# Kernel tuning notes

Hardware: AMD Instinct MI355X
Metric: run time of the kernel (lower is better)

## Reference

```python
import jax, jax.numpy as jnp
import numpy as np

B, K, S, H = 2, 16, 1024, 256
FFN_RATIO = 1.5
D_IN = 3 * H                      # concat of head/tail/context
D_FF = int(D_IN * FFN_RATIO)      # 1152
NEG_INF = -jnp.inf


def setup_inputs() -> dict:
    key = jax.random.key(0)
    ks = jax.random.split(key, 8)
    cand_span_reps = jax.random.normal(ks[0], (B, K, H), dtype=jnp.float32)
    # spans with start < end, leaving room so many pairs have a 'between' gap
    starts = jax.random.randint(ks[1], (B, K), 0, S - 8)
    widths = jax.random.randint(ks[2], (B, K), 1, 6)
    cand_span_ids = jnp.stack([starts, starts + widths], axis=-1).astype(jnp.int64)
    token_reps = jax.random.normal(ks[3], (B, S, H), dtype=jnp.float32)
    token_masks = jnp.ones((B, S), dtype=bool)
    rel_masks = jnp.ones((B, K * K), dtype=bool)
    # FFNProjectionLayer params: Linear(3H -> D_FF) + ReLU + Dropout(0) + Linear(D_FF -> H)
    W1 = jax.random.normal(ks[4], (D_IN, D_FF), dtype=jnp.float32) / np.sqrt(D_IN)
    b1 = jnp.zeros((D_FF,), dtype=jnp.float32)
    W2 = jax.random.normal(ks[5], (D_FF, H), dtype=jnp.float32) / np.sqrt(D_FF)
    b2 = jnp.zeros((H,), dtype=jnp.float32)
    return dict(cand_span_reps=cand_span_reps, cand_span_ids=cand_span_ids,
                token_reps=token_reps, token_masks=token_masks, rel_masks=rel_masks,
                W1=W1, b1=b1, W2=W2, b2=b2)


def reference(cand_span_reps, cand_span_ids, token_reps, token_masks, rel_masks,
              W1, b1, W2, b2):
    b, k, h = cand_span_reps.shape
    s = token_reps.shape[1]
    head = jnp.broadcast_to(cand_span_reps[:, :, None, :], (b, k, k, h))
    tail = jnp.broadcast_to(cand_span_reps[:, None, :, :], (b, k, k, h))
    hs = cand_span_ids[:, :, 0][:, :, None]   # (b,k,1)
    he = cand_span_ids[:, :, 1][:, :, None]
    ts = cand_span_ids[:, :, 0][:, None, :]   # (b,1,k)
    te = cand_span_ids[:, :, 1][:, None, :]
    min_end = jnp.minimum(he, te)              # (b,k,k)
    max_start = jnp.maximum(hs, ts)
    valid_between = (min_end < max_start) & rel_masks.reshape(b, k, k)
    seq = jnp.arange(s)
    # (b,k,k,s) dynamic-range mask: tokens in [min_end, max_start)
    mask = ((seq[None, None, None, :] >= min_end[..., None]) &
            (seq[None, None, None, :] < max_start[..., None]) &
            valid_between[..., None] &
            token_masks[:, None, None, :])
    # (b,k,k,s,h) masked tensor, max-pool over tokens (matches torch masked_fill+max)
    masked = jnp.where(mask[..., None], token_reps[:, None, None, :, :], NEG_INF)
    ctx = jnp.max(masked, axis=3)
    # replace all-masked (-inf) pairs with 0 to keep outputs finite
    ctx = jnp.where(mask.any(axis=3)[..., None], ctx, 0.0)
    rel = jnp.concatenate([head, tail, ctx], axis=-1)        # (b,k,k,3h)
    hid = jax.nn.relu(rel @ W1 + b1)                          # dropout p=0 -> identity
    out = hid @ W2 + b2                                       # (b,k,k,h)
    return out.reshape(b, k * k, h)
```

## Files before the change

### kernel.cpp

```cpp
#include <hip/hip_runtime.h>
#include <hip/hip_bf16.h>
#include <float.h>

#define BB 2
#define KK 16
#define SS 1024
#define HH 256
#define D_IN 768
#define D_FF 1152
#define NPAIR (BB*KK*KK)

#define CH 16
#define NCH (SS/CH)

typedef __attribute__((ext_vector_type(8))) short short8;
typedef __attribute__((ext_vector_type(4))) float floatx4;

__device__ __forceinline__ unsigned short f2bf(float f) {
    union { float f; unsigned u; } v; v.f = f;
    unsigned r = v.u + 0x7fffu + ((v.u >> 16) & 1u);
    return (unsigned short)(r >> 16);
}
__device__ __forceinline__ float bf2f(unsigned short s) {
    union { unsigned u; float f; } v; v.u = ((unsigned)s) << 16;
    return v.f;
}

__device__ __forceinline__ float rmax_f32(const float* __restrict__ p, int n)
{
    float m0 = -FLT_MAX, m1 = -FLT_MAX, m2 = -FLT_MAX, m3 = -FLT_MAX;
    int t = 0;
    for (; t + 4 <= n; t += 4) {
        float a = p[(size_t)(t + 0) * HH];
        float b = p[(size_t)(t + 1) * HH];
        float c = p[(size_t)(t + 2) * HH];
        float d = p[(size_t)(t + 3) * HH];
        m0 = fmaxf(m0, a); m1 = fmaxf(m1, b);
        m2 = fmaxf(m2, c); m3 = fmaxf(m3, d);
    }
    for (; t < n; ++t) m0 = fmaxf(m0, p[(size_t)t * HH]);
    return fmaxf(fmaxf(m0, m1), fmaxf(m2, m3));
}
__device__ __forceinline__ float rmax_bf16(const unsigned short* __restrict__ p, int n)
{
    float m0 = -FLT_MAX, m1 = -FLT_MAX, m2 = -FLT_MAX, m3 = -FLT_MAX;
    int t = 0;
    for (; t + 4 <= n; t += 4) {
        float a = bf2f(p[(size_t)(t + 0) * HH]);
        float b = bf2f(p[(size_t)(t + 1) * HH]);
        float c = bf2f(p[(size_t)(t + 2) * HH]);
        float d = bf2f(p[(size_t)(t + 3) * HH]);
        m0 = fmaxf(m0, a); m1 = fmaxf(m1, b);
        m2 = fmaxf(m2, c); m3 = fmaxf(m3, d);
    }
    for (; t < n; ++t) m0 = fmaxf(m0, bf2f(p[(size_t)t * HH]));
    return fmaxf(fmaxf(m0, m1), fmaxf(m2, m3));
}

#define W1_TILES (24*36)
#define W2_TILES (36*8)
#define PREP_BLOCKS (W1_TILES + W2_TILES + BB*NCH)
__global__ void prep_kernel(const float* __restrict__ W1, unsigned short* __restrict__ Wt1,
                            const float* __restrict__ W2, unsigned short* __restrict__ Wt2,
                            const float* __restrict__ tok, unsigned short* __restrict__ cmax)
{
    int bid = blockIdx.x;
    if (bid < W1_TILES + W2_TILES) {
        __shared__ unsigned short t[32][33];
        const float* W; unsigned short* Wt; int Kd, Nd, tk, tn;
        if (bid < W1_TILES) { W = W1; Wt = Wt1; Kd = D_IN;  Nd = D_FF; tk = bid / 36; tn = bid % 36; }
        else { bid -= W1_TILES; W = W2; Wt = Wt2; Kd = D_FF; Nd = HH;  tk = bid / 8;  tn = bid % 8; }
        const int r = threadIdx.x >> 5;
        const int c = threadIdx.x & 31;
        #pragma unroll
        for (int rr = r; rr < 32; rr += 8)
            t[rr][c] = f2bf(W[(size_t)(tk * 32 + rr) * Nd + tn * 32 + c]);
        __syncthreads();
        #pragma unroll
        for (int rr = r; rr < 32; rr += 8)
            Wt[(size_t)(tn * 32 + rr) * Kd + tk * 32 + c] = t[c][rr];
    } else {
        bid -= W1_TILES + W2_TILES;
        const int b = bid >> 6;
        const int c = bid & 63;
        const int h = threadIdx.x;
        const float* p = tok + ((size_t)(b * SS + c * CH)) * HH + h;
        float m0 = -FLT_MAX, m1 = -FLT_MAX, m2 = -FLT_MAX, m3 = -FLT_MAX;
        #pragma unroll
        for (int t = 0; t < CH; t += 4) {
            float a  = p[(size_t)(t + 0) * HH];
            float bb = p[(size_t)(t + 1) * HH];
            float cc = p[(size_t)(t + 2) * HH];
            float d  = p[(size_t)(t + 3) * HH];
            m0 = fmaxf(m0, a); m1 = fmaxf(m1, bb);
            m2 = fmaxf(m2, cc); m3 = fmaxf(m3, d);
        }
        cmax[(size_t)(b * NCH + c) * HH + h] = f2bf(fmaxf(fmaxf(m0, m1), fmaxf(m2, m3)));
    }
}

__global__ void build_x_kernel(const float* __restrict__ reps,
                               const int*   __restrict__ ids,
                               const float* __restrict__ tok,
                               const unsigned short* __restrict__ cmax,
                               unsigned short* __restrict__ X)
{
    const int p = blockIdx.x;
    const int h = threadIdx.x;
    const int b = p >> 8;
    const int i = (p >> 4) & 15;
    const int j = p & 15;

    const bool is64 = (ids[1] == 0);
    int hs, he, ts, te;
    if (is64) {
        hs = ids[((b*KK + i)*2 + 0) * 2];
        he = ids[((b*KK + i)*2 + 1) * 2];
        ts = ids[((b*KK + j)*2 + 0) * 2];
        te = ids[((b*KK + j)*2 + 1) * 2];
    } else {
        hs = ids[(b*KK + i)*2 + 0];
        he = ids[(b*KK + i)*2 + 1];
        ts = ids[(b*KK + j)*2 + 0];
        te = ids[(b*KK + j)*2 + 1];
    }

    const int lo = min(he, te);
    const int hi = max(hs, ts);

    const float head = reps[(size_t)(b*KK + i)*HH + h];
    const float tail = reps[(size_t)(b*KK + j)*HH + h];

    float m;
    if (lo < hi) {
        const float* trow = tok  + (size_t)b * SS  * HH + h;
        const unsigned short* crow = cmax + (size_t)b * NCH * HH + h;
        const int csta = (lo + CH - 1) >> 4;
        const int cend = hi >> 4;
        if (csta < cend) {
            float mA = rmax_f32(trow + (size_t)lo * HH, csta * CH - lo);
            float mB = rmax_bf16(crow + (size_t)csta * HH, cend - csta);
            float mC = rmax_f32(trow + (size_t)(cend * CH) * HH, hi - cend * CH);
            m = fmaxf(fmaxf(mA, mB), mC);
        } else {
            m = rmax_f32(trow + (size_t)lo * HH, hi - lo);
        }
    } else {
        m = 0.0f;
    }

    unsigned short* xr = X + (size_t)p * D_IN;
    xr[h]        = f2bf(head);
    xr[HH + h]   = f2bf(tail);
    xr[2*HH + h] = f2bf(m);
}

__global__ __launch_bounds__(256)
void gemm1_kernel(const unsigned short* __restrict__ A,
                  const unsigned short* __restrict__ Bt,
                  const float* __restrict__ bias,
                  unsigned short* __restrict__ C)
{
    constexpr int K = D_IN, N = D_FF, BK = 64, LDKT = BK + 8;
    __shared__ unsigned short As[64 * LDKT];
    __shared__ unsigned short Bs[64 * LDKT];

    const int tid  = threadIdx.x;
    const int lane = tid & 63;
    const int wave = tid >> 6;
    const int wm   = wave & 1;
    const int wn   = wave >> 1;
    const int quad = lane >> 4;
    const int l16  = lane & 15;

    const int rowBase = blockIdx.y * 64;
    const int colBase = blockIdx.x * 64;

    int srow[2], scol[2];
    #pragma unroll
    for (int s = 0; s < 2; ++s) {
        const int lin = tid * 2 + s;
        srow[s] = lin >> 3;
        scol[s] = (lin & 7) * 8;
    }

    floatx4 acc00 = {0.f,0.f,0.f,0.f}, acc01 = acc00, acc10 = acc00, acc11 = acc00;

    short8 pa[2], pb[2];
    #pragma unroll
    for (int s = 0; s < 2; ++s) {
        pa[s] = *(const short8*)&A [(size_t)(rowBase + srow[s]) * K + scol[s]];
        pb[s] = *(const short8*)&Bt[(size_t)(colBase + srow[s]) * K + scol[s]];
    }

    for (int k0 = 0; k0 < K; k0 += BK) {
        #pragma unroll
        for (int s = 0; s < 2; ++s) {
            *(short8*)&As[srow[s] * LDKT + scol[s]] = pa[s];
            *(short8*)&Bs[srow[s] * LDKT + scol[s]] = pb[s];
        }
        __syncthreads();

        const int kn = k0 + BK;
        if (kn < K) {
            #pragma unroll
            for (int s = 0; s < 2; ++s) {
                pa[s] = *(const short8*)&A [(size_t)(rowBase + srow[s]) * K + kn + scol[s]];
                pb[s] = *(const short8*)&Bt[(size_t)(colBase + srow[s]) * K + kn + scol[s]];
            }
        }

        #pragma unroll
        for (int kk = 0; kk < 2; ++kk) {
            const int ko = kk * 32 + quad * 8;
            short8 a0 = *(const short8*)&As[(wm * 32      + l16) * LDKT + ko];
            short8 a1 = *(const short8*)&As[(wm * 32 + 16 + l16) * LDKT + ko];
            short8 b0 = *(const short8*)&Bs[(wn * 32      + l16) * LDKT + ko];
            short8 b1 = *(const short8*)&Bs[(wn * 32 + 16 + l16) * LDKT + ko];
            acc00 = __builtin_amdgcn_mfma_f32_16x16x32_bf16(a0, b0, acc00, 0, 0, 0);
            acc01 = __builtin_amdgcn_mfma_f32_16x16x32_bf16(a0, b1, acc01, 0, 0, 0);
            acc10 = __builtin_amdgcn_mfma_f32_16x16x32_bf16(a1, b0, acc10, 0, 0, 0);
            acc11 = __builtin_amdgcn_mfma_f32_16x16x32_bf16(a1, b1, acc11, 0, 0, 0);
        }
        __syncthreads();
    }

    floatx4 accs[2][2] = {{acc00, acc01}, {acc10, acc11}};
    #pragma unroll
    for (int mt = 0; mt < 2; ++mt)
        #pragma unroll
        for (int nt = 0; nt < 2; ++nt)
            #pragma unroll
            for (int r = 0; r < 4; ++r) {
                const int m = rowBase + wm * 32 + mt * 16 + quad * 4 + r;
                const int n = colBase + wn * 32 + nt * 16 + l16;
                float v = fmaxf(accs[mt][nt][r] + bias[n], 0.0f);
                C[(size_t)m * N + n] = f2bf(v);
            }
}

__global__ __launch_bounds__(256)
void gemm2_kernel(const unsigned short* __restrict__ A,
                  const unsigned short* __restrict__ Bt,
                  const float* __restrict__ bias,
                  float* __restrict__ C)
{
    constexpr int K = D_FF, N = HH, BK = 64, LDKT = BK + 8;
    __shared__ unsigned short As[32 * LDKT];
    __shared__ unsigned short Bs[32 * LDKT];

    const int tid  = threadIdx.x;
    const int lane = tid & 63;
    const int wave = tid >> 6;
    const int wm   = wave & 1;
    const int wn   = wave >> 1;
    const int quad = lane >> 4;
    const int l16  = lane & 15;

    const int rowBase = blockIdx.y * 32;
    const int colBase = blockIdx.x * 32;

    const int srow = tid >> 3;
    const int scol = (tid & 7) * 8;

    floatx4 acc = {0.f,0.f,0.f,0.f};

    short8 pa = *(const short8*)&A [(size_t)(rowBase + srow) * K + scol];
    short8 pb = *(const short8*)&Bt[(size_t)(colBase + srow) * K + scol];

    for (int k0 = 0; k0 < K; k0 += BK) {
        *(short8*)&As[srow * LDKT + scol] = pa;
        *(short8*)&Bs[srow * LDKT + scol] = pb;
        __syncthreads();

        const int kn = k0 + BK;
        if (kn < K) {
            pa = *(const short8*)&A [(size_t)(rowBase + srow) * K + kn + scol];
            pb = *(const short8*)&Bt[(size_t)(colBase + srow) * K + kn + scol];
        }

        #pragma unroll
        for (int kk = 0; kk < 2; ++kk) {
            const int ko = kk * 32 + quad * 8;
            short8 a = *(const short8*)&As[(wm * 16 + l16) * LDKT + ko];
            short8 b = *(const short8*)&Bs[(wn * 16 + l16) * LDKT + ko];
            acc = __builtin_amdgcn_mfma_f32_16x16x32_bf16(a, b, acc, 0, 0, 0);
        }
        __syncthreads();
    }

    #pragma unroll
    for (int r = 0; r < 4; ++r) {
        const int m = rowBase + wm * 16 + quad * 4 + r;
        const int n = colBase + wn * 16 + l16;
        C[(size_t)m * N + n] = acc[r] + bias[n];
    }
}

extern "C" void kernel_launch(void* const* d_in, const int* in_sizes, int n_in,
                              void* d_out, int out_size, void* d_ws, size_t ws_size,
                              hipStream_t stream)
{
    const float* reps = (const float*)d_in[0];
    const int*   ids  = (const int*)  d_in[1];
    const float* tok  = (const float*)d_in[2];
    const float* W1   = (const float*)d_in[5];
    const float* b1   = (const float*)d_in[6];
    const float* W2   = (const float*)d_in[7];
    const float* b2   = (const float*)d_in[8];
    float* out = (float*)d_out;

    char* wsb = (char*)d_ws;
    unsigned short* Wt1  = (unsigned short*)(wsb);
    unsigned short* Wt2  = (unsigned short*)(wsb + 1769472);
    unsigned short* cmax = (unsigned short*)(wsb + 2359296);
    unsigned short* X    = (unsigned short*)(wsb + 2424832);
    unsigned short* hid  = (unsigned short*)(wsb + 3211264);

    prep_kernel<<<PREP_BLOCKS, 256, 0, stream>>>(W1, Wt1, W2, Wt2, tok, cmax);

    build_x_kernel<<<NPAIR, HH, 0, stream>>>(reps, ids, tok, cmax, X);

    gemm1_kernel<<<dim3(D_FF / 64, NPAIR / 64), 256, 0, stream>>>(X, Wt1, b1, hid);

    gemm2_kernel<<<dim3(HH / 32, NPAIR / 32), 256, 0, stream>>>(hid, Wt2, b2, out);
}
```

Measured before the change: 100.6 us.

## Fuse prep, build, and both GEMMs into one cooperative persistent kernel

Replaces the four separate launches (weight transpose and token chunk-max, pair feature build, GEMM1, GEMM2) with a single cooperative kernel of 512 blocks. The stages are separated by grid-wide syncs, and each block loops over its share of the prep jobs. This removes the launch overhead and inter-kernel gaps between stages. The max-reduction helpers are also widened to eight independent accumulators for more memory-level parallelism. The costs are the grid.sync barriers, idle blocks in the GEMM phases, and a dependence on cooperative launch residency.

```diff
diff --git a/kernel.cpp b/kernel.cpp
--- a/kernel.cpp
+++ b/kernel.cpp
@@ -1,6 +1,9 @@
 #include <hip/hip_runtime.h>
 #include <hip/hip_bf16.h>
+#include <hip/hip_cooperative_groups.h>
 #include <float.h>
+
+namespace cg = cooperative_groups;
 
 #define BB 2
 #define KK 16
@@ -13,6 +16,12 @@
 #define CH 16
 #define NCH (SS/CH)
 
+#define W1_TILES (24*36)
+#define W2_TILES (36*8)
+#define NJOBS (W1_TILES + W2_TILES + BB*NCH)
+
+#define GRID_BLOCKS 512
+
 typedef __attribute__((ext_vector_type(8))) short short8;
 typedef __attribute__((ext_vector_type(4))) float floatx4;
 
@@ -26,274 +35,268 @@
     return v.f;
 }
 
-__device__ __forceinline__ float rmax_f32(const float* __restrict__ p, int n)
+__device__ __forceinline__ float rmax8_f32(const float* __restrict__ p, int n)
 {
-    float m0 = -FLT_MAX, m1 = -FLT_MAX, m2 = -FLT_MAX, m3 = -FLT_MAX;
+    float m0=-FLT_MAX,m1=-FLT_MAX,m2=-FLT_MAX,m3=-FLT_MAX,
+          m4=-FLT_MAX,m5=-FLT_MAX,m6=-FLT_MAX,m7=-FLT_MAX;
     int t = 0;
-    for (; t + 4 <= n; t += 4) {
-        float a = p[(size_t)(t + 0) * HH];
-        float b = p[(size_t)(t + 1) * HH];
-        float c = p[(size_t)(t + 2) * HH];
-        float d = p[(size_t)(t + 3) * HH];
-        m0 = fmaxf(m0, a); m1 = fmaxf(m1, b);
-        m2 = fmaxf(m2, c); m3 = fmaxf(m3, d);
-    }
-    for (; t < n; ++t) m0 = fmaxf(m0, p[(size_t)t * HH]);
-    return fmaxf(fmaxf(m0, m1), fmaxf(m2, m3));
-}
-__device__ __forceinline__ float rmax_bf16(const unsigned short* __restrict__ p, int n)
+    for (; t + 8 <= n; t += 8) {
+        float v0=p[(size_t)(t+0)*HH], v1=p[(size_t)(t+1)*HH];
+        float v2=p[(size_t)(t+2)*HH], v3=p[(size_t)(t+3)*HH];
+        float v4=p[(size_t)(t+4)*HH], v5=p[(size_t)(t+5)*HH];
+        float v6=p[(size_t)(t+6)*HH], v7=p[(size_t)(t+7)*HH];
+        m0=fmaxf(m0,v0); m1=fmaxf(m1,v1); m2=fmaxf(m2,v2); m3=fmaxf(m3,v3);
+        m4=fmaxf(m4,v4); m5=fmaxf(m5,v5); m6=fmaxf(m6,v6); m7=fmaxf(m7,v7);
+    }
+    for (; t < n; ++t) m0 = fmaxf(m0, p[(size_t)t*HH]);
+    m0=fmaxf(m0,m1); m2=fmaxf(m2,m3); m4=fmaxf(m4,m5); m6=fmaxf(m6,m7);
+    return fmaxf(fmaxf(m0,m2), fmaxf(m4,m6));
+}
+__device__ __forceinline__ float rmax8_bf16(const unsigned short* __restrict__ p, int n)
 {
-    float m0 = -FLT_MAX, m1 = -FLT_MAX, m2 = -FLT_MAX, m3 = -FLT_MAX;
+    float m0=-FLT_MAX,m1=-FLT_MAX,m2=-FLT_MAX,m3=-FLT_MAX,
+          m4=-FLT_MAX,m5=-FLT_MAX,m6=-FLT_MAX,m7=-FLT_MAX;
     int t = 0;
-    for (; t + 4 <= n; t += 4) {
-        float a = bf2f(p[(size_t)(t + 0) * HH]);
-        float b = bf2f(p[(size_t)(t + 1) * HH]);
-        float c = bf2f(p[(size_t)(t + 2) * HH]);
-        float d = bf2f(p[(size_t)(t + 3) * HH]);
-        m0 = fmaxf(m0, a); m1 = fmaxf(m1, b);
-        m2 = fmaxf(m2, c); m3 = fmaxf(m3, d);
-    }
-    for (; t < n; ++t) m0 = fmaxf(m0, bf2f(p[(size_t)t * HH]));
-    return fmaxf(fmaxf(m0, m1), fmaxf(m2, m3));
-}
-
-#define W1_TILES (24*36)
-#define W2_TILES (36*8)
-#define PREP_BLOCKS (W1_TILES + W2_TILES + BB*NCH)
-__global__ void prep_kernel(const float* __restrict__ W1, unsigned short* __restrict__ Wt1,
-                            const float* __restrict__ W2, unsigned short* __restrict__ Wt2,
-                            const float* __restrict__ tok, unsigned short* __restrict__ cmax)
+    for (; t + 8 <= n; t += 8) {
+        float v0=bf2f(p[(size_t)(t+0)*HH]), v1=bf2f(p[(size_t)(t+1)*HH]);
+        float v2=bf2f(p[(size_t)(t+2)*HH]), v3=bf2f(p[(size_t)(t+3)*HH]);
+        float v4=bf2f(p[(size_t)(t+4)*HH]), v5=bf2f(p[(size_t)(t+5)*HH]);
+        float v6=bf2f(p[(size_t)(t+6)*HH]), v7=bf2f(p[(size_t)(t+7)*HH]);
+        m0=fmaxf(m0,v0); m1=fmaxf(m1,v1); m2=fmaxf(m2,v2); m3=fmaxf(m3,v3);
+        m4=fmaxf(m4,v4); m5=fmaxf(m5,v5); m6=fmaxf(m6,v6); m7=fmaxf(m7,v7);
+    }
+    for (; t < n; ++t) m0 = fmaxf(m0, bf2f(p[(size_t)t*HH]));
+    m0=fmaxf(m0,m1); m2=fmaxf(m2,m3); m4=fmaxf(m4,m5); m6=fmaxf(m6,m7);
+    return fmaxf(fmaxf(m0,m2), fmaxf(m4,m6));
+}
+
+__global__ __launch_bounds__(256, 2)
+void mega_kernel(const float* __restrict__ W1, const float* __restrict__ W2,
+                 const float* __restrict__ tok, const float* __restrict__ reps,
+                 const int* __restrict__ ids,
+                 const float* __restrict__ b1, const float* __restrict__ b2,
+                 unsigned short* __restrict__ Wt1, unsigned short* __restrict__ Wt2,
+                 unsigned short* __restrict__ cmax, unsigned short* __restrict__ X,
+                 unsigned short* __restrict__ hid, float* __restrict__ out)
 {
-    int bid = blockIdx.x;
-    if (bid < W1_TILES + W2_TILES) {
-        __shared__ unsigned short t[32][33];
-        const float* W; unsigned short* Wt; int Kd, Nd, tk, tn;
-        if (bid < W1_TILES) { W = W1; Wt = Wt1; Kd = D_IN;  Nd = D_FF; tk = bid / 36; tn = bid % 36; }
-        else { bid -= W1_TILES; W = W2; Wt = Wt2; Kd = D_FF; Nd = HH;  tk = bid / 8;  tn = bid % 8; }
-        const int r = threadIdx.x >> 5;
-        const int c = threadIdx.x & 31;
-        #pragma unroll
-        for (int rr = r; rr < 32; rr += 8)
-            t[rr][c] = f2bf(W[(size_t)(tk * 32 + rr) * Nd + tn * 32 + c]);
-        __syncthreads();
-        #pragma unroll
-        for (int rr = r; rr < 32; rr += 8)
-            Wt[(size_t)(tn * 32 + rr) * Kd + tk * 32 + c] = t[c][rr];
-    } else {
-        bid -= W1_TILES + W2_TILES;
-        const int b = bid >> 6;
-        const int c = bid & 63;
-        const int h = threadIdx.x;
-        const float* p = tok + ((size_t)(b * SS + c * CH)) * HH + h;
-        float m0 = -FLT_MAX, m1 = -FLT_MAX, m2 = -FLT_MAX, m3 = -FLT_MAX;
-        #pragma unroll
-        for (int t = 0; t < CH; t += 4) {
-            float a  = p[(size_t)(t + 0) * HH];
-            float bb = p[(size_t)(t + 1) * HH];
-            float cc = p[(size_t)(t + 2) * HH];
-            float d  = p[(size_t)(t + 3) * HH];
-            m0 = fmaxf(m0, a); m1 = fmaxf(m1, bb);
-            m2 = fmaxf(m2, cc); m3 = fmaxf(m3, d);
-        }
-        cmax[(size_t)(b * NCH + c) * HH + h] = f2bf(fmaxf(fmaxf(m0, m1), fmaxf(m2, m3)));
-    }
-}
-
-__global__ void build_x_kernel(const float* __restrict__ reps,
-                               const int*   __restrict__ ids,
-                               const float* __restrict__ tok,
-                               const unsigned short* __restrict__ cmax,
-                               unsigned short* __restrict__ X)
-{
-    const int p = blockIdx.x;
-    const int h = threadIdx.x;
-    const int b = p >> 8;
-    const int i = (p >> 4) & 15;
-    const int j = p & 15;
-
-    const bool is64 = (ids[1] == 0);
-    int hs, he, ts, te;
-    if (is64) {
-        hs = ids[((b*KK + i)*2 + 0) * 2];
-        he = ids[((b*KK + i)*2 + 1) * 2];
-        ts = ids[((b*KK + j)*2 + 0) * 2];
-        te = ids[((b*KK + j)*2 + 1) * 2];
-    } else {
-        hs = ids[(b*KK + i)*2 + 0];
-        he = ids[(b*KK + i)*2 + 1];
-        ts = ids[(b*KK + j)*2 + 0];
-        te = ids[(b*KK + j)*2 + 1];
-    }
-
-    const int lo = min(he, te);
-    const int hi = max(hs, ts);
-
-    const float head = reps[(size_t)(b*KK + i)*HH + h];
-    const float tail = reps[(size_t)(b*KK + j)*HH + h];
-
-    float m;
-    if (lo < hi) {
-        const float* trow = tok  + (size_t)b * SS  * HH + h;
-        const unsigned short* crow = cmax + (size_t)b * NCH * HH + h;
-        const int csta = (lo + CH - 1) >> 4;
-        const int cend = hi >> 4;
-        if (csta < cend) {
-            float mA = rmax_f32(trow + (size_t)lo * HH, csta * CH - lo);
-            float mB = rmax_bf16(crow + (size_t)csta * HH, cend - csta);
-            float mC = rmax_f32(trow + (size_t)(cend * CH) * HH, hi - cend * CH);
-            m = fmaxf(fmaxf(mA, mB), mC);
-        } else {
-            m = rmax_f32(trow + (size_t)lo * HH, hi - lo);
-        }
-    } else {
-        m = 0.0f;
-    }
-
-    unsigned short* xr = X + (size_t)p * D_IN;
-    xr[h]        = f2bf(head);
-    xr[HH + h]   = f2bf(tail);
-    xr[2*HH + h] = f2bf(m);
-}
-
-__global__ __launch_bounds__(256)
-void gemm1_kernel(const unsigned short* __restrict__ A,
-                  const unsigned short* __restrict__ Bt,
-                  const float* __restrict__ bias,
-                  unsigned short* __restrict__ C)
-{
-    constexpr int K = D_IN, N = D_FF, BK = 64, LDKT = BK + 8;
-    __shared__ unsigned short As[64 * LDKT];
-    __shared__ unsigned short Bs[64 * LDKT];
-
-    const int tid  = threadIdx.x;
+    cg::grid_group grid = cg::this_grid();
+    __shared__ unsigned short smem[2 * 64 * 72];
+
+    const int bid = blockIdx.x;
+    const int tid = threadIdx.x;
     const int lane = tid & 63;
     const int wave = tid >> 6;
-    const int wm   = wave & 1;
-    const int wn   = wave >> 1;
     const int quad = lane >> 4;
     const int l16  = lane & 15;
 
-    const int rowBase = blockIdx.y * 64;
-    const int colBase = blockIdx.x * 64;
-
-    int srow[2], scol[2];
-    #pragma unroll
-    for (int s = 0; s < 2; ++s) {
-        const int lin = tid * 2 + s;
-        srow[s] = lin >> 3;
-        scol[s] = (lin & 7) * 8;
-    }
-
-    floatx4 acc00 = {0.f,0.f,0.f,0.f}, acc01 = acc00, acc10 = acc00, acc11 = acc00;
-
-    short8 pa[2], pb[2];
-    #pragma unroll
-    for (int s = 0; s < 2; ++s) {
-        pa[s] = *(const short8*)&A [(size_t)(rowBase + srow[s]) * K + scol[s]];
-        pb[s] = *(const short8*)&Bt[(size_t)(colBase + srow[s]) * K + scol[s]];
-    }
-
-    for (int k0 = 0; k0 < K; k0 += BK) {
+    for (int job = bid; job < NJOBS; job += GRID_BLOCKS) {
+        if (job < W1_TILES + W2_TILES) {
+            int jb = job;
+            const float* W; unsigned short* Wt; int Kd, Nd, tk, tn;
+            if (jb < W1_TILES) { W = W1; Wt = Wt1; Kd = D_IN;  Nd = D_FF; tk = jb / 36; tn = jb % 36; }
+            else { jb -= W1_TILES; W = W2; Wt = Wt2; Kd = D_FF; Nd = HH;  tk = jb / 8;  tn = jb % 8; }
+            unsigned short (*t)[33] = (unsigned short(*)[33])smem;
+            const int r = tid >> 5;
+            const int c = tid & 31;
+            #pragma unroll
+            for (int rr = r; rr < 32; rr += 8)
+                t[rr][c] = f2bf(W[(size_t)(tk * 32 + rr) * Nd + tn * 32 + c]);
+            __syncthreads();
+            #pragma unroll
+            for (int rr = r; rr < 32; rr += 8)
+                Wt[(size_t)(tn * 32 + rr) * Kd + tk * 32 + c] = t[c][rr];
+            __syncthreads();
+        } else {
+            const int jb = job - (W1_TILES + W2_TILES);
+            const int b = jb >> 6;
+            const int c = jb & 63;
+            const float* p = tok + ((size_t)(b * SS + c * CH)) * HH + tid;
+            float m0=-FLT_MAX,m1=-FLT_MAX,m2=-FLT_MAX,m3=-FLT_MAX;
+            #pragma unroll
+            for (int t = 0; t < CH; t += 4) {
+                float a  = p[(size_t)(t+0)*HH];
+                float bb = p[(size_t)(t+1)*HH];
+                float cc = p[(size_t)(t+2)*HH];
+                float d  = p[(size_t)(t+3)*HH];
+                m0=fmaxf(m0,a); m1=fmaxf(m1,bb); m2=fmaxf(m2,cc); m3=fmaxf(m3,d);
+            }
+            cmax[(size_t)(b * NCH + c) * HH + tid] =
+                f2bf(fmaxf(fmaxf(m0,m1), fmaxf(m2,m3)));
+        }
+    }
+
+    grid.sync();
+
+    {
+        const int p = bid;
+        const int b = p >> 8;
+        const int i = (p >> 4) & 15;
+        const int j = p & 15;
+        const int h = tid;
+
+        const bool is64 = (ids[1] == 0);
+        int hs, he, ts, te;
+        if (is64) {
+            hs = ids[((b*KK + i)*2 + 0) * 2];
+            he = ids[((b*KK + i)*2 + 1) * 2];
+            ts = ids[((b*KK + j)*2 + 0) * 2];
+            te = ids[((b*KK + j)*2 + 1) * 2];
+        } else {
+            hs = ids[(b*KK + i)*2 + 0];
+            he = ids[(b*KK + i)*2 + 1];
+            ts = ids[(b*KK + j)*2 + 0];
+            te = ids[(b*KK + j)*2 + 1];
+        }
+        const int lo = min(he, te);
+        const int hi = max(hs, ts);
+
+        const float head = reps[(size_t)(b*KK + i)*HH + h];
+        const float tail = reps[(size_t)(b*KK + j)*HH + h];
+
+        float m;
+        if (lo < hi) {
+            const float* trow = tok  + (size_t)b * SS  * HH + h;
+            const unsigned short* crow = cmax + (size_t)b * NCH * HH + h;
+            const int csta = (lo + CH - 1) >> 4;
+            const int cend = hi >> 4;
+            if (csta < cend) {
+                float mA = rmax8_f32(trow + (size_t)lo * HH, csta * CH - lo);
+                float mB = rmax8_bf16(crow + (size_t)csta * HH, cend - csta);
+                float mC = rmax8_f32(trow + (size_t)(cend * CH) * HH, hi - cend * CH);
+                m = fmaxf(fmaxf(mA, mB), mC);
+            } else {
+                m = rmax8_f32(trow + (size_t)lo * HH, hi - lo);
+            }
+        } else {
+            m = 0.0f;
+        }
+
+        unsigned short* xr = X + (size_t)p * D_IN;
+        xr[h]        = f2bf(head);
+        xr[HH + h]   = f2bf(tail);
+        xr[2*HH + h] = f2bf(m);
+    }
+
+    grid.sync();
+
+    if (bid < (D_FF/64) * (NPAIR/64)) {
+        constexpr int K = D_IN, N = D_FF, BK = 64, LDKT = BK + 8;
+        unsigned short* As = smem;
+        unsigned short* Bs = smem + 64 * LDKT;
+        const int wm = wave & 1;
+        const int wn = wave >> 1;
+        const int rowBase = (bid / (D_FF/64)) * 64;
+        const int colBase = (bid % (D_FF/64)) * 64;
+
+        int srow[2], scol[2];
         #pragma unroll
         for (int s = 0; s < 2; ++s) {
-            *(short8*)&As[srow[s] * LDKT + scol[s]] = pa[s];
-            *(short8*)&Bs[srow[s] * LDKT + scol[s]] = pb[s];
-        }
-        __syncthreads();
-
-        const int kn = k0 + BK;
-        if (kn < K) {
+            const int lin = tid * 2 + s;
+            srow[s] = lin >> 3;
+            scol[s] = (lin & 7) * 8;
+        }
+
+        floatx4 acc00 = {0.f,0.f,0.f,0.f}, acc01 = acc00, acc10 = acc00, acc11 = acc00;
+
+        short8 pa[2], pb[2];
+        #pragma unroll
+        for (int s = 0; s < 2; ++s) {
+            pa[s] = *(const short8*)&X  [(size_t)(rowBase + srow[s]) * K + scol[s]];
+            pb[s] = *(const short8*)&Wt1[(size_t)(colBase + srow[s]) * K + scol[s]];
+        }
+
+        for (int k0 = 0; k0 < K; k0 += BK) {
             #pragma unroll
             for (int s = 0; s < 2; ++s) {
-                pa[s] = *(const short8*)&A [(size_t)(rowBase + srow[s]) * K + kn + scol[s]];
-                pb[s] = *(const short8*)&Bt[(size_t)(colBase + srow[s]) * K + kn + scol[s]];
-            }
-        }
-
+                *(short8*)&As[srow[s] * LDKT + scol[s]] = pa[s];
+                *(short8*)&Bs[srow[s] * LDKT + scol[s]] = pb[s];
+            }
+            __syncthreads();
+
+            const int kn = k0 + BK;
+            if (kn < K) {
+                #pragma unroll
+                for (int s = 0; s < 2; ++s) {
+                    pa[s] = *(const short8*)&X  [(size_t)(rowBase + srow[s]) * K + kn + scol[s]];
+                    pb[s] = *(const short8*)&Wt1[(size_t)(colBase + srow[s]) * K + kn + scol[s]];
+                }
+            }
+
+            #pragma unroll
+            for (int kk = 0; kk < 2; ++kk) {
+                const int ko = kk * 32 + quad * 8;
+                short8 a0 = *(const short8*)&As[(wm * 32      + l16) * LDKT + ko];
+                short8 a1 = *(const short8*)&As[(wm * 32 + 16 + l16) * LDKT + ko];
+                short8 b0 = *(const short8*)&Bs[(wn * 32      + l16) * LDKT + ko];
+                short8 b1 = *(const short8*)&Bs[(wn * 32 + 16 + l16) * LDKT + ko];
+                acc00 = __builtin_amdgcn_mfma_f32_16x16x32_bf16(a0, b0, acc00, 0, 0, 0);
+                acc01 = __builtin_amdgcn_mfma_f32_16x16x32_bf16(a0, b1, acc01, 0, 0, 0);
+                acc10 = __builtin_amdgcn_mfma_f32_16x16x32_bf16(a1, b0, acc10, 0, 0, 0);
+                acc11 = __builtin_amdgcn_mfma_f32_16x16x32_bf16(a1, b1, acc11, 0, 0, 0);
+            }
+            __syncthreads();
+        }
+
+        floatx4 accs[2][2] = {{acc00, acc01}, {acc10, acc11}};
         #pragma unroll
-        for (int kk = 0; kk < 2; ++kk) {
-            const int ko = kk * 32 + quad * 8;
-            short8 a0 = *(const short8*)&As[(wm * 32      + l16) * LDKT + ko];
-            short8 a1 = *(const short8*)&As[(wm * 32 + 16 + l16) * LDKT + ko];
-            short8 b0 = *(const short8*)&Bs[(wn * 32      + l16) * LDKT + ko];
-            short8 b1 = *(const short8*)&Bs[(wn * 32 + 16 + l16) * LDKT + ko];
-            acc00 = __builtin_amdgcn_mfma_f32_16x16x32_bf16(a0, b0, acc00, 0, 0, 0);
-            acc01 = __builtin_amdgcn_mfma_f32_16x16x32_bf16(a0, b1, acc01, 0, 0, 0);
-            acc10 = __builtin_amdgcn_mfma_f32_16x16x32_bf16(a1, b0, acc10, 0, 0, 0);
-            acc11 = __builtin_amdgcn_mfma_f32_16x16x32_bf16(a1, b1, acc11, 0, 0, 0);
-        }
-        __syncthreads();
-    }
-
-    floatx4 accs[2][2] = {{acc00, acc01}, {acc10, acc11}};
-    #pragma unroll
-    for (int mt = 0; mt < 2; ++mt)
+        for (int mt = 0; mt < 2; ++mt)
+            #pragma unroll
+            for (int nt = 0; nt < 2; ++nt)
+                #pragma unroll
+                for (int r = 0; r < 4; ++r) {
+                    const int m = rowBase + wm * 32 + mt * 16 + quad * 4 + r;
+                    const int n = colBase + wn * 32 + nt * 16 + l16;
+                    float v = fmaxf(accs[mt][nt][r] + b1[n], 0.0f);
+                    hid[(size_t)m * N + n] = f2bf(v);
+                }
+    }
+
+    grid.sync();
+
+    if (bid < (HH/32) * (NPAIR/32)) {
+        constexpr int K = D_FF, N = HH, BK = 64, LDKT = BK + 8;
+        unsigned short* As = smem;
+        unsigned short* Bs = smem + 32 * LDKT;
+        const int wm = wave & 1;
+        const int wn = wave >> 1;
+        const int rowBase = (bid / (HH/32)) * 32;
+        const int colBase = (bid % (HH/32)) * 32;
+
+        const int srow = tid >> 3;
+        const int scol = (tid & 7) * 8;
+
+        floatx4 acc = {0.f,0.f,0.f,0.f};
+
+        short8 pa = *(const short8*)&hid[(size_t)(rowBase + srow) * K + scol];
+        short8 pb = *(const short8*)&Wt2[(size_t)(colBase + srow) * K + scol];
+
+        for (int k0 = 0; k0 < K; k0 += BK) {
+            *(short8*)&As[srow * LDKT + scol] = pa;
+            *(short8*)&Bs[srow * LDKT + scol] = pb;
+            __syncthreads();
+
+            const int kn = k0 + BK;
+            if (kn < K) {
+                pa = *(const short8*)&hid[(size_t)(rowBase + srow) * K + kn + scol];
+                pb = *(const short8*)&Wt2[(size_t)(colBase + srow) * K + kn + scol];
+            }
+
+            #pragma unroll
+            for (int kk = 0; kk < 2; ++kk) {
+                const int ko = kk * 32 + quad * 8;
+                short8 a = *(const short8*)&As[(wm * 16 + l16) * LDKT + ko];
+                short8 b = *(const short8*)&Bs[(wn * 16 + l16) * LDKT + ko];
+                acc = __builtin_amdgcn_mfma_f32_16x16x32_bf16(a, b, acc, 0, 0, 0);
+            }
+            __syncthreads();
+        }
+
         #pragma unroll
-        for (int nt = 0; nt < 2; ++nt)
-            #pragma unroll
-            for (int r = 0; r < 4; ++r) {
-                const int m = rowBase + wm * 32 + mt * 16 + quad * 4 + r;
-                const int n = colBase + wn * 32 + nt * 16 + l16;
-                float v = fmaxf(accs[mt][nt][r] + bias[n], 0.0f);
-                C[(size_t)m * N + n] = f2bf(v);
-            }
-}
-
-__global__ __launch_bounds__(256)
-void gemm2_kernel(const unsigned short* __restrict__ A,
-                  const unsigned short* __restrict__ Bt,
-                  const float* __restrict__ bias,
-                  float* __restrict__ C)
-{
-    constexpr int K = D_FF, N = HH, BK = 64, LDKT = BK + 8;
-    __shared__ unsigned short As[32 * LDKT];
-    __shared__ unsigned short Bs[32 * LDKT];
-
-    const int tid  = threadIdx.x;
-    const int lane = tid & 63;
-    const int wave = tid >> 6;
-    const int wm   = wave & 1;
-    const int wn   = wave >> 1;
-    const int quad = lane >> 4;
-    const int l16  = lane & 15;
-
-    const int rowBase = blockIdx.y * 32;
-    const int colBase = blockIdx.x * 32;
-
-    const int srow = tid >> 3;
-    const int scol = (tid & 7) * 8;
-
-    floatx4 acc = {0.f,0.f,0.f,0.f};
-
-    short8 pa = *(const short8*)&A [(size_t)(rowBase + srow) * K + scol];
-    short8 pb = *(const short8*)&Bt[(size_t)(colBase + srow) * K + scol];
-
-    for (int k0 = 0; k0 < K; k0 += BK) {
-        *(short8*)&As[srow * LDKT + scol] = pa;
-        *(short8*)&Bs[srow * LDKT + scol] = pb;
-        __syncthreads();
-
-        const int kn = k0 + BK;
-        if (kn < K) {
-            pa = *(const short8*)&A [(size_t)(rowBase + srow) * K + kn + scol];
-            pb = *(const short8*)&Bt[(size_t)(colBase + srow) * K + kn + scol];
-        }
-
-        #pragma unroll
-        for (int kk = 0; kk < 2; ++kk) {
-            const int ko = kk * 32 + quad * 8;
-            short8 a = *(const short8*)&As[(wm * 16 + l16) * LDKT + ko];
-            short8 b = *(const short8*)&Bs[(wn * 16 + l16) * LDKT + ko];
-            acc = __builtin_amdgcn_mfma_f32_16x16x32_bf16(a, b, acc, 0, 0, 0);
-        }
-        __syncthreads();
-    }
-
-    #pragma unroll
-    for (int r = 0; r < 4; ++r) {
-        const int m = rowBase + wm * 16 + quad * 4 + r;
-        const int n = colBase + wn * 16 + l16;
-        C[(size_t)m * N + n] = acc[r] + bias[n];
+        for (int r = 0; r < 4; ++r) {
+            const int m = rowBase + wm * 16 + quad * 4 + r;
+            const int n = colBase + wn * 16 + l16;
+            out[(size_t)m * N + n] = acc[r] + b2[n];
+        }
     }
 }
 
@@ -317,11 +320,12 @@
     unsigned short* X    = (unsigned short*)(wsb + 2424832);
     unsigned short* hid  = (unsigned short*)(wsb + 3211264);
 
-    prep_kernel<<<PREP_BLOCKS, 256, 0, stream>>>(W1, Wt1, W2, Wt2, tok, cmax);
-
-    build_x_kernel<<<NPAIR, HH, 0, stream>>>(reps, ids, tok, cmax, X);
-
-    gemm1_kernel<<<dim3(D_FF / 64, NPAIR / 64), 256, 0, stream>>>(X, Wt1, b1, hid);
-
-    gemm2_kernel<<<dim3(HH / 32, NPAIR / 32), 256, 0, stream>>>(hid, Wt2, b2, out);
-}
+    void* args[] = {
+        (void*)&W1, (void*)&W2, (void*)&tok, (void*)&reps, (void*)&ids,
+        (void*)&b1, (void*)&b2,
+        (void*)&Wt1, (void*)&Wt2, (void*)&cmax, (void*)&X, (void*)&hid,
+        (void*)&out
+    };
+    hipLaunchCooperativeKernel((const void*)mega_kernel,
+                               dim3(GRID_BLOCKS), dim3(256), args, 0, stream);
+}
```

New measurement: 295.3 us. 193% more time.
